# Kernel tuning notes

Hardware: AMD Instinct MI355X
Metric: run time of the kernel (lower is better)

## Reference

```python
import jax, jax.numpy as jnp
import numpy as np

INPUT_SIZE = 28
NUM_RPS = 5
RP_SIZE = 72
NET = NUM_RPS * RP_SIZE  # 360
NUM_CLASSES = 10
LEAK = 0.95
LN_EPS = 1e-5


def setup_inputs() -> dict:
    key = jax.random.key(0)
    ks = jax.random.split(key, 12)
    B, T = 4096, 64
    x = jax.random.normal(ks[0], (B, T, INPUT_SIZE), dtype=jnp.float32)
    sc_in = 1.0 / np.sqrt(INPUT_SIZE)
    sc_net = 1.0 / np.sqrt(NET)
    return {
        "x": x,
        "reasoning_steps": 16,
        "W_in": jax.random.normal(ks[1], (NET, INPUT_SIZE), dtype=jnp.float32) * sc_in,
        "b_in": jnp.zeros((NET,), dtype=jnp.float32),
        "W_gate": jax.random.normal(ks[2], (NET, INPUT_SIZE), dtype=jnp.float32) * sc_in,
        "b_gate": jnp.zeros((NET,), dtype=jnp.float32),
        "W_rec": jax.random.normal(ks[3], (NET, NET), dtype=jnp.float32) * sc_net,
        "ln_gamma": jnp.ones((NET,), dtype=jnp.float32),
        "ln_beta": jnp.zeros((NET,), dtype=jnp.float32),
        "threshold": jax.random.normal(ks[4], (NET,), dtype=jnp.float32),
        "intrinsic": jax.random.normal(ks[5], (NET,), dtype=jnp.float32),
        "steepness": jnp.full((NET,), 5.0, dtype=jnp.float32),
        "reset_scale": jnp.full((NET,), 0.5, dtype=jnp.float32),
        "W_cls": jax.random.normal(ks[6], (NUM_CLASSES, NET), dtype=jnp.float32) * sc_net,
        "b_cls": jnp.zeros((NUM_CLASSES,), dtype=jnp.float32),
    }


def _layer_norm(h, gamma, beta):
    mu = jnp.mean(h, axis=-1, keepdims=True)
    var = jnp.mean(jnp.square(h - mu), axis=-1, keepdims=True)
    return (h - mu) * jax.lax.rsqrt(var + LN_EPS) * gamma + beta


def _neuron_step(total_current, potential, threshold, intrinsic, steepness, reset_scale):
    # PulseTGAU: leak, integrate, soft-gated spike, partial reset.
    potential = potential * LEAK + total_current + intrinsic
    gp = potential - threshold
    sg = jax.nn.sigmoid(gp * jnp.abs(steepness))
    out = jax.nn.silu(gp) * sg
    potential = potential - reset_scale * (gp * sg)
    return out, potential


def reference(x, reasoning_steps, W_in, b_in, W_gate, b_gate, W_rec,
              ln_gamma, ln_beta, threshold, intrinsic, steepness, reset_scale,
              W_cls, b_cls):
    B = x.shape[0]
    # Precompute gated input signal for all timesteps: [B, T, NET]
    gate = jax.nn.sigmoid(jnp.einsum('btf,nf->btn', x, W_gate) + b_gate)
    ginp = (jnp.einsum('btf,nf->btn', x, W_in) + b_in) * gate  # gated input
    ginp_t = jnp.swapaxes(ginp, 0, 1)  # [T, B, NET]

    def cell(carry, gated_input):
        spikes, potential = carry
        cur = gated_input + spikes @ W_rec.T
        cur = _layer_norm(cur, ln_gamma, ln_beta)
        spikes, potential = _neuron_step(cur, potential, threshold, intrinsic,
                                         steepness, reset_scale)
        return (spikes, potential), None

    init = (jnp.zeros((B, NET), x.dtype), jnp.zeros((B, NET), x.dtype))
    carry, _ = jax.lax.scan(cell, init, ginp_t)

    def reason(carry, _):
        spikes, potential = carry
        cur = _layer_norm(spikes @ W_rec.T, ln_gamma, ln_beta)
        spikes, potential = _neuron_step(cur, potential, threshold, intrinsic,
                                         steepness, reset_scale)
        return (spikes, potential), None

    carry, _ = jax.lax.scan(reason, carry, None, length=reasoning_steps)
    spikes, _ = carry
    return spikes @ W_cls.T + b_cls
```

## Files before the change

### kernel.cpp

```cpp
#include <hip/hip_runtime.h>
#include <math.h>


#define NET    360
#define NPAD   384
#define K8N    48
#define RPB    16
#define NBLK   256
#define NTHR   512
#define NTILE  3

typedef _Float16 f16x8 __attribute__((ext_vector_type(8)));
typedef float    f32x4 __attribute__((ext_vector_type(4)));

#define WREC_E (K8N * NPAD * 8)
#define WIN_E  (4 * NPAD * 8)

__global__ void prep_kernel(const float* __restrict__ W_rec,
                            const float* __restrict__ W_in,
                            const float* __restrict__ W_gate,
                            _Float16* __restrict__ Bh, _Float16* __restrict__ Bl,
                            _Float16* __restrict__ Wio)
{
    int idx = blockIdx.x * 256 + threadIdx.x;
    if (idx < WREC_E) {
        int k8 = idx / (NPAD * 8), rem = idx % (NPAD * 8);
        int n = rem >> 3, j = rem & 7, k = k8 * 8 + j;
        float v = (k < NET && n < NET) ? W_rec[n * NET + k] : 0.f;
        _Float16 h = (_Float16)v;
        Bh[idx] = h; Bl[idx] = (_Float16)(v - (float)h);
    } else if (idx < WREC_E + 2 * WIN_E) {
        int e = idx - WREC_E;
        int which = e / WIN_E;
        int f = e % WIN_E;
        int k8 = f / (NPAD * 8), rem = f % (NPAD * 8);
        int n = rem >> 3, j = rem & 7, k = k8 * 8 + j;
        const float* W = which ? W_gate : W_in;
        float v = (k < 28 && n < NET) ? W[n * 28 + k] : 0.f;
        _Float16 h = (_Float16)v;
        Wio[(2 * which) * WIN_E + f]     = h;
        Wio[(2 * which + 1) * WIN_E + f] = (_Float16)(v - (float)h);
    }
}

__device__ __forceinline__ float sigm(float v) {
    return __builtin_amdgcn_rcpf(1.f + __expf(-v));
}

__global__ __launch_bounds__(NTHR, 2)
void resonator_kernel(const float* __restrict__ x,
                      const int*   __restrict__ rsteps_p,
                      const float* __restrict__ b_in,
                      const float* __restrict__ b_gate,
                      const float* __restrict__ ln_g,
                      const float* __restrict__ ln_b,
                      const float* __restrict__ thr_p,
                      const float* __restrict__ intr_p,
                      const float* __restrict__ steep_p,
                      const float* __restrict__ reset_p,
                      const float* __restrict__ W_cls,
                      const float* __restrict__ b_cls,
                      const _Float16* __restrict__ Bh_g,
                      const _Float16* __restrict__ Bl_g,
                      const _Float16* __restrict__ Wio_g,
                      float* __restrict__ out)
{
    __shared__ __align__(16) _Float16 Ah[K8N * RPB * 8];
    __shared__ __align__(16) _Float16 xbuf[2][4 * RPB * 8];
    __shared__ __align__(16) _Float16 Bc[8 * 12 * 64 * 8];
    __shared__ __align__(16) _Float16 Wl[8 * 2 * 3 * 64 * 8];
    __shared__ float red[8][33];

    const int tid  = threadIdx.x;
    const int w    = tid >> 6;
    const int lane = tid & 63;
    const int quad = lane >> 4;
    const int l15  = lane & 15;
    const int row0 = blockIdx.x * RPB;

    float gam[NTILE], bet[NTILE], thrv[NTILE], intv[NTILE], asp[NTILE], rscv[NTILE],
          binv[NTILE], bgtv[NTILE];
#pragma unroll
    for (int i = 0; i < NTILE; ++i) {
        int n_i = (w * NTILE + i) * 16 + l15;
        bool a = n_i < NET;
        gam[i]  = a ? ln_g[n_i]   : 0.f;
        bet[i]  = a ? ln_b[n_i]   : 0.f;
        thrv[i] = a ? thr_p[n_i]  : 0.f;
        intv[i] = a ? intr_p[n_i] : 0.f;
        asp[i]  = a ? fabsf(steep_p[n_i]) : 0.f;
        rscv[i] = a ? reset_p[n_i] : 0.f;
        binv[i] = a ? b_in[n_i]   : 0.f;
        bgtv[i] = a ? b_gate[n_i] : 0.f;
    }

    float pot[NTILE][4];
#pragma unroll
    for (int i = 0; i < NTILE; ++i)
#pragma unroll
        for (int r = 0; r < 4; ++r) pot[i][r] = 0.f;

    for (int e = tid; e < K8N * RPB * 8; e += NTHR) Ah[e] = (_Float16)0.f;
    for (int e = tid; e < 2 * 4 * RPB * 8; e += NTHR) ((_Float16*)xbuf)[e] = (_Float16)0.f;
    __syncthreads();

    const f16x8* Bph = (const f16x8*)Bh_g;
    const f16x8* Aph = (const f16x8*)Ah;
    const f16x8* Wp  = (const f16x8*)Wio_g;
    f16x8* Bcv = (f16x8*)Bc;
    f16x8* Wlv = (f16x8*)Wl;
    const int bb = quad * NPAD + w * (NTILE * 16) + l15;

    f16x8 rbh[6][NTILE];
#pragma unroll
    for (int kt = 0; kt < 6; ++kt)
#pragma unroll
        for (int i = 0; i < NTILE; ++i)
            rbh[kt][i] = Bph[bb + i * 16 + kt * (4 * NPAD)];
#pragma unroll
    for (int kt = 6; kt < 10; ++kt)
#pragma unroll
        for (int i = 0; i < NTILE; ++i)
            Bcv[(w * 12 + (kt - 6) * 3 + i) * 64 + lane] = Bph[bb + i * 16 + kt * (4 * NPAD)];

#pragma unroll
    for (int which = 0; which < 2; ++which)
#pragma unroll
        for (int i = 0; i < NTILE; ++i)
            Wlv[((w * 2 + which) * 3 + i) * 64 + lane] =
                Wp[(which * 2) * (WIN_E / 8) + bb + i * 16];

    const bool xact = tid < RPB * 28;
    const int  xm   = tid / 28;
    const int  xf   = tid - xm * 28;
    const int  xix  = ((xf >> 3) * RPB + xm) * 8 + (xf & 7);
    const float* xsrc = x + ((size_t)(row0 + xm) * 64) * 28 + xf;

    if (xact) xbuf[0][xix] = (_Float16)xsrc[0];

    const int Ttot = 64 + *rsteps_p;

    for (int t = 0; t < Ttot; ++t) {
        __syncthreads();

        f32x4 acc[NTILE];
#pragma unroll
        for (int i = 0; i < NTILE; ++i) acc[i] = (f32x4){0.f, 0.f, 0.f, 0.f};

#pragma unroll
        for (int kt = 0; kt < 6; ++kt) {
            f16x8 ah = Aph[lane + kt * 64];
#pragma unroll
            for (int i = 0; i < NTILE; ++i)
                acc[i] = __builtin_amdgcn_mfma_f32_16x16x32_f16(ah, rbh[kt][i], acc[i], 0, 0, 0);
        }
#pragma unroll
        for (int kt = 6; kt < 10; ++kt) {
            f16x8 ah = Aph[lane + kt * 64];
#pragma unroll
            for (int i = 0; i < NTILE; ++i) {
                f16x8 bh = Bcv[(w * 12 + (kt - 6) * 3 + i) * 64 + lane];
                acc[i] = __builtin_amdgcn_mfma_f32_16x16x32_f16(ah, bh, acc[i], 0, 0, 0);
            }
        }
#pragma unroll
        for (int q = 10; q < 12; ++q) {
            f16x8 ah = Aph[lane + q * 64];
#pragma unroll
            for (int i = 0; i < NTILE; ++i) {
                f16x8 bh = Bph[bb + i * 16 + q * (4 * NPAD)];
                acc[i] = __builtin_amdgcn_mfma_f32_16x16x32_f16(ah, bh, acc[i], 0, 0, 0);
            }
        }

        if (t < 64) {
            const f16x8* Xh = (const f16x8*)xbuf[t & 1];
            f16x8 xa = Xh[lane];
#pragma unroll
            for (int i = 0; i < NTILE; ++i) {
                f16x8 ih = Wlv[((w * 2 + 0) * 3 + i) * 64 + lane];
                f16x8 gh = Wlv[((w * 2 + 1) * 3 + i) * 64 + lane];
                f32x4 ia = (f32x4){binv[i], binv[i], binv[i], binv[i]};
                f32x4 ga = (f32x4){bgtv[i], bgtv[i], bgtv[i], bgtv[i]};
                ia = __builtin_amdgcn_mfma_f32_16x16x32_f16(xa, ih, ia, 0, 0, 0);
                ga = __builtin_amdgcn_mfma_f32_16x16x32_f16(xa, gh, ga, 0, 0, 0);
#pragma unroll
                for (int r = 0; r < 4; ++r) acc[i][r] += ia[r] * sigm(ga[r]);
            }
        }

        if (t < 63 && xact) xbuf[(t + 1) & 1][xix] = (_Float16)xsrc[(t + 1) * 28];

#pragma unroll
        for (int r = 0; r < 4; ++r) {
            float v  = acc[0][r] + acc[1][r] + acc[2][r];
            float v2 = acc[0][r] * acc[0][r] + acc[1][r] * acc[1][r] + acc[2][r] * acc[2][r];
#pragma unroll
            for (int off = 1; off < 16; off <<= 1) {
                v  += __shfl_xor(v,  off);
                v2 += __shfl_xor(v2, off);
            }
            if (l15 == 0) {
                red[w][(quad * 4 + r) * 2]     = v;
                red[w][(quad * 4 + r) * 2 + 1] = v2;
            }
        }

        __syncthreads();

        float mu_r[4], rs_r[4];
#pragma unroll
        for (int r = 0; r < 4; ++r) {
            int row2 = (quad * 4 + r) * 2;
            float val = red[l15 & 7][row2 + (l15 >> 3)];
            val += __shfl_xor(val, 1);
            val += __shfl_xor(val, 2);
            val += __shfl_xor(val, 4);
            float other = __shfl_xor(val, 8);
            float S  = (l15 < 8) ? val : other;
            float S2 = (l15 < 8) ? other : val;
            float mu = S * (1.f / NET);
            mu_r[r] = mu;
            rs_r[r] = __builtin_amdgcn_rsqf(S2 * (1.f / NET) - mu * mu + 1e-5f);
        }

#pragma unroll
        for (int i = 0; i < NTILE; ++i) {
            int n_i  = (w * NTILE + i) * 16 + l15;
            int base = ((n_i >> 3) * RPB) * 8 + (n_i & 7);
#pragma unroll
            for (int r = 0; r < 4; ++r) {
                int m = quad * 4 + r;
                float cur = (acc[i][r] - mu_r[r]) * rs_r[r] * gam[i] + bet[i];
                float p   = pot[i][r] * 0.95f + cur + intv[i];
                float gp  = p - thrv[i];
                float sg  = sigm(gp * asp[i]);
                float sp  = sigm(gp);
                float gsg = gp * sg;
                float o   = gsg * sp;
                pot[i][r] = p - rscv[i] * gsg;
                Ah[base + m * 8] = (_Float16)o;
            }
        }
    }

    __syncthreads();
    if (tid < RPB * 10 * 2) {
        int p = tid >> 1, chunk = tid & 1;
        int r = p / 10, c = p - r * 10;
        const float* wc = W_cls + c * NET;
        float s = chunk ? 0.f : b_cls[c];
        int k0 = chunk * 180;
        for (int k = k0; k < k0 + 180; ++k) {
            int ix = ((k >> 3) * RPB + r) * 8 + (k & 7);
            s = fmaf((float)Ah[ix], wc[k], s);
        }
        float other = __shfl_down(s, 1);
        if (!chunk) out[(size_t)(row0 + r) * 10 + c] = s + other;
    }
}

extern "C" void kernel_launch(void* const* d_in, const int* in_sizes, int n_in,
                              void* d_out, int out_size, void* d_ws, size_t ws_size,
                              hipStream_t stream)
{
    const float* x      = (const float*)d_in[0];
    const int*   rsteps = (const int*)  d_in[1];
    const float* W_in   = (const float*)d_in[2];
    const float* b_in   = (const float*)d_in[3];
    const float* W_gate = (const float*)d_in[4];
    const float* b_gate = (const float*)d_in[5];
    const float* W_rec  = (const float*)d_in[6];
    const float* ln_g   = (const float*)d_in[7];
    const float* ln_b   = (const float*)d_in[8];
    const float* thr    = (const float*)d_in[9];
    const float* intr   = (const float*)d_in[10];
    const float* steep  = (const float*)d_in[11];
    const float* rsc    = (const float*)d_in[12];
    const float* W_cls  = (const float*)d_in[13];
    const float* b_cls  = (const float*)d_in[14];
    float*       out    = (float*)d_out;

    _Float16* Bh  = (_Float16*)d_ws;
    _Float16* Bl  = Bh + WREC_E;
    _Float16* Wio = Bl + WREC_E;

    const int total = WREC_E + 2 * WIN_E;
    prep_kernel<<<dim3((total + 255) / 256), dim3(256), 0, stream>>>(
        W_rec, W_in, W_gate, Bh, Bl, Wio);
    resonator_kernel<<<dim3(NBLK), dim3(NTHR), 0, stream>>>(
        x, rsteps, b_in, b_gate, ln_g, ln_b, thr, intr, steep, rsc,
        W_cls, b_cls, Bh, Bl, Wio, out);
}
```

Measured before the change: 371.5 us.

## Spread recurrent matmul over twelve waves with two column tiles each

Raises the block from 8 to 12 waves, so each wave owns 2 instead of 3 16-column output tiles of the 384-wide recurrent product. The LDS slice of the recurrent weights and the layer-norm reduction are resized to match. The gated-input weight staging in LDS is dropped, and those weights are now read from global memory every timestep. The intent is more wave parallelism and less per-wave MFMA and register work, at the cost of more wave sync and reduction traffic and extra global loads per step.

```diff
diff --git a/kernel.cpp b/kernel.cpp
--- a/kernel.cpp
+++ b/kernel.cpp
@@ -7,8 +7,9 @@
 #define K8N    48
 #define RPB    16
 #define NBLK   256
-#define NTHR   512
-#define NTILE  3
+#define NTHR   768
+#define NW     12
+#define NTILE  2
 
 typedef _Float16 f16x8 __attribute__((ext_vector_type(8)));
 typedef float    f32x4 __attribute__((ext_vector_type(4)));
@@ -47,7 +48,8 @@
     return __builtin_amdgcn_rcpf(1.f + __expf(-v));
 }
 
-__global__ __launch_bounds__(NTHR, 2)
+__global__ __launch_bounds__(NTHR)
+__attribute__((amdgpu_waves_per_eu(3, 3)))
 void resonator_kernel(const float* __restrict__ x,
                       const int*   __restrict__ rsteps_p,
                       const float* __restrict__ b_in,
@@ -67,9 +69,8 @@
 {
     __shared__ __align__(16) _Float16 Ah[K8N * RPB * 8];
     __shared__ __align__(16) _Float16 xbuf[2][4 * RPB * 8];
-    __shared__ __align__(16) _Float16 Bc[8 * 12 * 64 * 8];
-    __shared__ __align__(16) _Float16 Wl[8 * 2 * 3 * 64 * 8];
-    __shared__ float red[8][33];
+    __shared__ __align__(16) _Float16 Bc[NW * 8 * 64 * 8];
+    __shared__ float red[NW][33];
 
     const int tid  = threadIdx.x;
     const int w    = tid >> 6;
@@ -108,7 +109,6 @@
     const f16x8* Aph = (const f16x8*)Ah;
     const f16x8* Wp  = (const f16x8*)Wio_g;
     f16x8* Bcv = (f16x8*)Bc;
-    f16x8* Wlv = (f16x8*)Wl;
     const int bb = quad * NPAD + w * (NTILE * 16) + l15;
 
     f16x8 rbh[6][NTILE];
@@ -121,14 +121,7 @@
     for (int kt = 6; kt < 10; ++kt)
 #pragma unroll
         for (int i = 0; i < NTILE; ++i)
-            Bcv[(w * 12 + (kt - 6) * 3 + i) * 64 + lane] = Bph[bb + i * 16 + kt * (4 * NPAD)];
-
-#pragma unroll
-    for (int which = 0; which < 2; ++which)
-#pragma unroll
-        for (int i = 0; i < NTILE; ++i)
-            Wlv[((w * 2 + which) * 3 + i) * 64 + lane] =
-                Wp[(which * 2) * (WIN_E / 8) + bb + i * 16];
+            Bcv[(w * 8 + (kt - 6) * 2 + i) * 64 + lane] = Bph[bb + i * 16 + kt * (4 * NPAD)];
 
     const bool xact = tid < RPB * 28;
     const int  xm   = tid / 28;
@@ -159,7 +152,7 @@
             f16x8 ah = Aph[lane + kt * 64];
 #pragma unroll
             for (int i = 0; i < NTILE; ++i) {
-                f16x8 bh = Bcv[(w * 12 + (kt - 6) * 3 + i) * 64 + lane];
+                f16x8 bh = Bcv[(w * 8 + (kt - 6) * 2 + i) * 64 + lane];
                 acc[i] = __builtin_amdgcn_mfma_f32_16x16x32_f16(ah, bh, acc[i], 0, 0, 0);
             }
         }
@@ -178,8 +171,8 @@
             f16x8 xa = Xh[lane];
 #pragma unroll
             for (int i = 0; i < NTILE; ++i) {
-                f16x8 ih = Wlv[((w * 2 + 0) * 3 + i) * 64 + lane];
-                f16x8 gh = Wlv[((w * 2 + 1) * 3 + i) * 64 + lane];
+                f16x8 ih = Wp[0 * (WIN_E / 8) + bb + i * 16];
+                f16x8 gh = Wp[2 * (WIN_E / 8) + bb + i * 16];
                 f32x4 ia = (f32x4){binv[i], binv[i], binv[i], binv[i]};
                 f32x4 ga = (f32x4){bgtv[i], bgtv[i], bgtv[i], bgtv[i]};
                 ia = __builtin_amdgcn_mfma_f32_16x16x32_f16(xa, ih, ia, 0, 0, 0);
@@ -193,8 +186,8 @@
 
 #pragma unroll
         for (int r = 0; r < 4; ++r) {
-            float v  = acc[0][r] + acc[1][r] + acc[2][r];
-            float v2 = acc[0][r] * acc[0][r] + acc[1][r] * acc[1][r] + acc[2][r] * acc[2][r];
+            float v  = acc[0][r] + acc[1][r];
+            float v2 = acc[0][r] * acc[0][r] + acc[1][r] * acc[1][r];
 #pragma unroll
             for (int off = 1; off < 16; off <<= 1) {
                 v  += __shfl_xor(v,  off);
@@ -211,8 +204,10 @@
         float mu_r[4], rs_r[4];
 #pragma unroll
         for (int r = 0; r < 4; ++r) {
-            int row2 = (quad * 4 + r) * 2;
-            float val = red[l15 & 7][row2 + (l15 >> 3)];
+            int idx = (quad * 4 + r) * 2 + (l15 >> 3);
+            int wv  = l15 & 7;
+            float val = red[wv][idx];
+            if (wv < 4) val += red[8 + wv][idx];
             val += __shfl_xor(val, 1);
             val += __shfl_xor(val, 2);
             val += __shfl_xor(val, 4);
```

New measurement: 396.8 us. 6.8% more time.
